# Kernel tuning notes

Measured on AMD Instinct MI355X. Metric: run time of the kernel, lower is better.

Reference implementation:

```python
import jax, jax.numpy as jnp
import numpy as np

B, S, HID = 2, 2048, 2048
NH, NKV, HD = 16, 4, 128
ROT = 64            # head_dim * partial_rotary_factor
WINDOW = 512        # sliding_window_size
ROPE_BASE = 10000.0


def setup_inputs() -> dict:
    key = jax.random.key(0)
    ks = jax.random.split(key, 5)
    scale = 0.02
    return {
        "hidden_states": jax.random.normal(ks[0], (B, S, HID), jnp.float32),
        "Wq": jax.random.normal(ks[1], (NH * HD, HID), jnp.float32) * scale,
        "Wk": jax.random.normal(ks[2], (NKV * HD, HID), jnp.float32) * scale,
        "Wv": jax.random.normal(ks[3], (NKV * HD, HID), jnp.float32) * scale,
        "Wo": jax.random.normal(ks[4], (HID, NH * HD), jnp.float32) * scale,
    }


def _rope_cos_sin(seq_len, dtype):
    inv_freq = 1.0 / (ROPE_BASE ** (jnp.arange(0, ROT, 2, dtype=jnp.float32) / ROT))
    t = jnp.arange(seq_len, dtype=jnp.float32)
    freqs = t[:, None] * inv_freq[None, :]          # [S, ROT/2]
    emb = jnp.concatenate([freqs, freqs], axis=-1)   # [S, ROT]
    return jnp.cos(emb).astype(dtype), jnp.sin(emb).astype(dtype)


def _rotate_half(x):
    x1, x2 = x[..., : x.shape[-1] // 2], x[..., x.shape[-1] // 2:]
    return jnp.concatenate([-x2, x1], axis=-1)


def reference(hidden_states, Wq, Wk, Wv, Wo):
    b, s, _ = hidden_states.shape
    n_rep = NH // NKV

    q = (hidden_states @ Wq.T).reshape(b, s, NH, HD).transpose(0, 2, 1, 3)    # [B,NH,S,HD]
    k = (hidden_states @ Wk.T).reshape(b, s, NKV, HD).transpose(0, 2, 1, 3)   # [B,NKV,S,HD]
    v = (hidden_states @ Wv.T).reshape(b, s, NKV, HD).transpose(0, 2, 1, 3)

    # partial rotary embedding on the first ROT dims
    cos, sin = _rope_cos_sin(s, q.dtype)   # [S, ROT]
    cos = cos[None, None]                  # broadcast over batch, heads
    sin = sin[None, None]
    q_rot, q_pass = q[..., :ROT], q[..., ROT:]
    k_rot, k_pass = k[..., :ROT], k[..., ROT:]
    q_rot = q_rot * cos + _rotate_half(q_rot) * sin
    k_rot = k_rot * cos + _rotate_half(k_rot) * sin
    q = jnp.concatenate([q_rot, q_pass], axis=-1)
    k = jnp.concatenate([k_rot, k_pass], axis=-1)

    # GQA: repeat kv heads
    k = jnp.repeat(k, n_rep, axis=1)   # [B,NH,S,HD]
    v = jnp.repeat(v, n_rep, axis=1)

    scores = jnp.einsum("bhqd,bhkd->bhqk", q, k) / jnp.sqrt(jnp.asarray(HD, q.dtype))

    # sliding-window causal mask: allow j in [i-WINDOW+1, i]
    i = jnp.arange(s)[:, None]
    j = jnp.arange(s)[None, :]
    allowed = (j <= i) & (j > i - WINDOW)
    scores = jnp.where(allowed[None, None], scores, -jnp.inf)

    attn = jax.nn.softmax(scores.astype(jnp.float32), axis=-1).astype(q.dtype)
    out = jnp.einsum("bhqk,bhkd->bhqd", attn, v)          # [B,NH,S,HD]
    out = out.transpose(0, 2, 1, 3).reshape(b, s, NH * HD)
    return out @ Wo.T
```

## Files before the change

### kernel.cpp

```cpp
#include <hip/hip_runtime.h>
#include <cstdint>
#include <cstddef>

typedef __bf16 bf16;
typedef __attribute__((ext_vector_type(8))) __bf16 bf16x8;
typedef __attribute__((ext_vector_type(4))) __bf16 bf16x4;
typedef __attribute__((ext_vector_type(4))) float f32x4;
typedef __attribute__((ext_vector_type(4))) short s16x4;

#define S_LEN   2048
#define WIN     512
#define NH_Q    16
#define NH_KV   4
#define HD_     128
#define NTOK    4096

#define QSCALE_LOG2E 0.12751744561823337f

#if defined(__has_builtin)
#if __has_builtin(__builtin_amdgcn_mfma_f32_16x16x16bf16_1k)
#define HAVE_MFMA16 1
#endif
#endif
#ifndef HAVE_MFMA16
#define HAVE_MFMA16 0
#endif

#define WAIT_VM4   0x0F74
#define WAIT_VM3   0x0F73
#define WAIT_VM2   0x0F72
#define WAIT_VM0   0x0F70
#define WAIT_L0    0xC07F
#define WAIT_L4    0xC47F
#define WAIT_L6    0xC67F
#define WAIT_L10   0xCA7F
#define CFENCE() __asm__ __volatile__("" ::: "memory")

__device__ __forceinline__ void async_copy16(const void* g, void* l) {
  __builtin_amdgcn_global_load_lds(
      (const __attribute__((address_space(1))) void*)g,
      (__attribute__((address_space(3))) void*)l, 16, 0, 0);
}

__global__ __launch_bounds__(256)
void cvt_all(const float* __restrict__ hs, const float* __restrict__ wq,
             const float* __restrict__ wk, const float* __restrict__ wv,
             const float* __restrict__ wo, bf16* __restrict__ hsb,
             bf16* __restrict__ wqb, bf16* __restrict__ wkb,
             bf16* __restrict__ wvb, bf16* __restrict__ wob) {
  long i = ((long)blockIdx.x * 256 + threadIdx.x) * 4;
  const float* in;
  bf16* out;
  if (i < 8388608)       { in = hs + i;            out = hsb + i; }
  else if (i < 12582912) { in = wq + (i - 8388608); out = wqb + (i - 8388608); }
  else if (i < 13631488) { in = wk + (i - 12582912); out = wkb + (i - 12582912); }
  else if (i < 14680064) { in = wv + (i - 13631488); out = wvb + (i - 13631488); }
  else                   { in = wo + (i - 14680064); out = wob + (i - 14680064); }
  float4 v = *(const float4*)in;
  bf16x4 t = {(bf16)v.x, (bf16)v.y, (bf16)v.z, (bf16)v.w};
  *(bf16x4*)out = t;
}

__global__ __launch_bounds__(512, 2)
void gemm_out8(const bf16* __restrict__ A, const bf16* __restrict__ W,
               float* __restrict__ C) {
  __shared__ __align__(16) char smem[98304];
  const int tid  = threadIdx.x;
  const int wave = tid >> 6, lane = tid & 63;
  const int quad = lane >> 4, l16 = lane & 15;
  const int wm = wave >> 1, wn = wave & 1;

  const int flat = blockIdx.y * 16 + blockIdx.x;
  const int swz  = (flat & 7) * 32 + (flat >> 3);
  const int m0 = (swz >> 4) * 256;
  const int n0 = (swz & 15) * 128;

  const int rdb = (l16 * 64 + quad * 16) ^ ((l16 & 8) << 2);
  const int srow = lane >> 2;
  const int scol = ((lane & 3) * 8) ^ ((lane >> 5) << 4);

  const bf16* aptr[2][2];
  int adst[2][2];
#pragma unroll
  for (int mh = 0; mh < 2; ++mh)
#pragma unroll
    for (int j = 0; j < 2; ++j) {
      const int rb = (wave >> 1) * 4 + mh * 2 + j;
      aptr[mh][j] = A + (size_t)(m0 + rb * 16 + srow) * 2048 + scol
                    + (wave & 1) * 32;
      adst[mh][j] = (rb * 2 + (wave & 1)) << 10;
    }
  const bf16* bptr[2];
  int bdst[2];
#pragma unroll
  for (int nh = 0; nh < 2; ++nh) {
    const int cb = (wave >> 2) * 4 + nh * 2 + ((wave >> 1) & 1);
    bptr[nh] = W + (size_t)(n0 + cb * 16 + srow) * 2048 + scol
               + (wave & 1) * 32;
    bdst[nh] = (cb * 2 + (wave & 1)) << 10;
  }

#define STAGE_A(mh, tt) do { char* _b = smem + ((tt) & 1) * 32768;      \
    async_copy16(aptr[mh][0] + (tt) * 64, _b + adst[mh][0]);            \
    async_copy16(aptr[mh][1] + (tt) * 64, _b + adst[mh][1]); } while (0)
#define STAGE_B(nh, tt) do { char* _b = smem + 65536 + ((tt) & 1) * 16384; \
    async_copy16(bptr[nh] + (tt) * 64, _b + bdst[nh]); } while (0)

  f32x4 acc[4][4];
#pragma unroll
  for (int i = 0; i < 4; ++i)
#pragma unroll
    for (int j = 0; j < 4; ++j) acc[i][j] = (f32x4){0.f, 0.f, 0.f, 0.f};

  bf16x8 afr[2][2];
  bf16x8 bfr[2][2][2];

  auto read_a = [&](const char* Ab, int mh) __attribute__((always_inline)) {
#pragma unroll
    for (int mt2 = 0; mt2 < 2; ++mt2)
#pragma unroll
      for (int ks = 0; ks < 2; ++ks)
        afr[mt2][ks] = *(const bf16x8*)(
            Ab + (((wm * 4 + mh * 2 + mt2) * 2 + ks) << 10) + rdb);
  };
  auto read_b = [&](const char* Bb, int nh) __attribute__((always_inline)) {
#pragma unroll
    for (int nt2 = 0; nt2 < 2; ++nt2)
#pragma unroll
      for (int ks = 0; ks < 2; ++ks)
        bfr[nh][nt2][ks] = *(const bf16x8*)(
            Bb + (((wn * 4 + nh * 2 + nt2) * 2 + ks) << 10) + rdb);
  };
  auto do_mfma = [&](int mh, int nh) __attribute__((always_inline)) {
    __builtin_amdgcn_s_setprio(1);
#pragma unroll
    for (int mt2 = 0; mt2 < 2; ++mt2)
#pragma unroll
      for (int nt2 = 0; nt2 < 2; ++nt2)
#pragma unroll
        for (int ks = 0; ks < 2; ++ks)
          acc[mh * 2 + mt2][nh * 2 + nt2] = __builtin_amdgcn_mfma_f32_16x16x32_bf16(
              afr[mt2][ks], bfr[nh][nt2][ks], acc[mh * 2 + mt2][nh * 2 + nt2],
              0, 0, 0);
    __builtin_amdgcn_s_setprio(0);
  };

  STAGE_A(0, 0); STAGE_B(0, 0); STAGE_B(1, 0); STAGE_A(1, 0);
  CFENCE();

  for (int t = 0; t < 31; ++t) {
    const char* Ab = smem + (t & 1) * 32768;
    const char* Bb = smem + 65536 + (t & 1) * 16384;
    const int nx = t + 1;
    __builtin_amdgcn_s_waitcnt(WAIT_VM3); CFENCE();
    __builtin_amdgcn_s_barrier(); CFENCE();
    read_a(Ab, 0); read_b(Bb, 0);
    STAGE_A(0, nx); CFENCE();
    do_mfma(0, 0);
    __builtin_amdgcn_s_waitcnt(WAIT_VM4); CFENCE();
    __builtin_amdgcn_s_barrier(); CFENCE();
    read_b(Bb, 1);
    STAGE_B(0, nx); CFENCE();
    do_mfma(0, 1);
    __builtin_amdgcn_s_waitcnt(WAIT_VM3); CFENCE();
    __builtin_amdgcn_s_barrier(); CFENCE();
    read_a(Ab, 1);
    STAGE_B(1, nx); CFENCE();
    do_mfma(1, 0);
    __builtin_amdgcn_s_barrier(); CFENCE();
    STAGE_A(1, nx); CFENCE();
    do_mfma(1, 1);
  }
  {
    const char* Ab = smem + 32768;
    const char* Bb = smem + 65536 + 16384;
    __builtin_amdgcn_s_waitcnt(WAIT_VM3); CFENCE();
    __builtin_amdgcn_s_barrier(); CFENCE();
    read_a(Ab, 0); read_b(Bb, 0);
    do_mfma(0, 0);
    __builtin_amdgcn_s_waitcnt(WAIT_VM2); CFENCE();
    __builtin_amdgcn_s_barrier(); CFENCE();
    read_b(Bb, 1);
    do_mfma(0, 1);
    __builtin_amdgcn_s_waitcnt(WAIT_VM0); CFENCE();
    __builtin_amdgcn_s_barrier(); CFENCE();
    read_a(Ab, 1);
    do_mfma(1, 0);
    do_mfma(1, 1);
  }
#undef STAGE_A
#undef STAGE_B

#pragma unroll
  for (int mt = 0; mt < 4; ++mt)
#pragma unroll
    for (int nt = 0; nt < 4; ++nt)
#pragma unroll
      for (int r = 0; r < 4; ++r) {
        const int row = m0 + wm * 64 + mt * 16 + quad * 4 + r;
        const int col = n0 + wn * 64 + nt * 16 + l16;
        C[(size_t)row * 2048 + col] = acc[mt][nt][r];
      }
}

__global__ __launch_bounds__(512, 2)
void gemm_qkv10(const bf16* __restrict__ A, const bf16* __restrict__ Wq,
                const bf16* __restrict__ Wk, const bf16* __restrict__ Wv,
                bf16* __restrict__ Qo, bf16* __restrict__ Ko,
                bf16* __restrict__ Vt) {
  __shared__ __align__(16) char smem[114688];
  const int tid  = threadIdx.x;
  const int wave = tid >> 6, lane = tid & 63;
  const int quad = lane >> 4, l16 = lane & 15;
  const int wm = wave >> 1, wn = wave & 1;

  const int flat = blockIdx.y * 16 + blockIdx.x;
  const int swz  = (flat & 7) * 32 + (flat >> 3);
  const int m0 = (swz >> 4) * 256;
  const int n0 = (swz & 15) * 192;

  const int rdb = (l16 * 64 + quad * 16) ^ ((l16 & 8) << 2);
  const int srow = lane >> 2;
  const int scol = ((lane & 3) * 8) ^ ((lane >> 5) << 4);

  const int rbA0 = (wave >> 1) * 4 + (wave & 1);
  const int rbA1 = rbA0 + 2;
  const bf16* a0p = A + (size_t)(m0 + rbA0 * 16 + srow) * 2048 + scol;
  const bf16* a1p = A + (size_t)(m0 + rbA1 * 16 + srow) * 2048 + scol;
  const int da0 = (rbA0 * 2) << 10;
  const int da1 = (rbA1 * 2) << 10;

  const int rbB0 = wave >> 1, khB0 = wave & 1;
  const int rbB1 = 4 + wave;
  const int nrow0 = n0 + rbB0 * 16 + srow;
  const int nrow1 = n0 + rbB1 * 16 + srow;
  const bf16* b0p = (nrow0 < 2048 ? Wq + (size_t)nrow0 * 2048
                   : nrow0 < 2560 ? Wk + (size_t)(nrow0 - 2048) * 2048
                                  : Wv + (size_t)(nrow0 - 2560) * 2048)
                    + scol + khB0 * 32;
  const bf16* b1p = (nrow1 < 2048 ? Wq + (size_t)nrow1 * 2048
                   : nrow1 < 2560 ? Wk + (size_t)(nrow1 - 2048) * 2048
                                  : Wv + (size_t)(nrow1 - 2560) * 2048)
                    + scol;
  const int db0 = (rbB0 * 2 + khB0) << 10;
  const int db1 = (rbB1 * 2) << 10;

#define STAGE_A0(tt) do { char* _b = smem + ((tt) & 1) * 32768;        \
    async_copy16(a0p + (tt) * 64,      _b + da0);                      \
    async_copy16(a0p + (tt) * 64 + 32, _b + da0 + 1024); } while (0)
#define STAGE_A1(tt) do { char* _b = smem + ((tt) & 1) * 32768;        \
    async_copy16(a1p + (tt) * 64,      _b + da1);                      \
    async_copy16(a1p + (tt) * 64 + 32, _b + da1 + 1024); } while (0)
#define STAGE_B0(tt) do { char* _b = smem + 65536 + ((tt) & 1) * 24576; \
    async_copy16(b0p + (tt) * 64,      _b + db0); } while (0)
#define STAGE_B12(tt) do { char* _b = smem + 65536 + ((tt) & 1) * 24576; \
    async_copy16(b1p + (tt) * 64,      _b + db1);                      \
    async_copy16(b1p + (tt) * 64 + 32, _b + db1 + 1024); } while (0)

  f32x4 acc[4][6];
#pragma unroll
  for (int i = 0; i < 4; ++i)
#pragma unroll
    for (int j = 0; j < 6; ++j) acc[i][j] = (f32x4){0.f, 0.f, 0.f, 0.f};

  bf16x8 afr0[2][2];
  bf16x8 afr1[2][2];
  bf16x8 bfr[6][2];

  auto read_a0 = [&](const char* Ab) __attribute__((always_inline)) {
#pragma unroll
    for (int mt2 = 0; mt2 < 2; ++mt2)
#pragma unroll
      for (int ks = 0; ks < 2; ++ks)
        afr0[mt2][ks] = *(const bf16x8*)(
            Ab + (((wm * 4 + mt2) * 2 + ks) << 10) + rdb);
  };
  auto read_a1 = [&](const char* Ab) __attribute__((always_inline)) {
#pragma unroll
    for (int mt2 = 0; mt2 < 2; ++mt2)
#pragma unroll
      for (int ks = 0; ks < 2; ++ks)
        afr1[mt2][ks] = *(const bf16x8*)(
            Ab + (((wm * 4 + 2 + mt2) * 2 + ks) << 10) + rdb);
  };
  auto read_b_ks = [&](const char* Bb, int ks) __attribute__((always_inline)) {
#pragma unroll
    for (int j = 0; j < 6; ++j) {
      const int cc = (j >> 1) * 4 + (j & 1) * 2 + wn;
      bfr[j][ks] = *(const bf16x8*)(Bb + ((cc * 2 + ks) << 10) + rdb);
    }
  };
  auto mfma0 = [&](int ks) __attribute__((always_inline)) {
    __builtin_amdgcn_s_setprio(1);
#pragma unroll
    for (int mt2 = 0; mt2 < 2; ++mt2)
#pragma unroll
      for (int j = 0; j < 6; ++j)
        acc[mt2][j] = __builtin_amdgcn_mfma_f32_16x16x32_bf16(
            afr0[mt2][ks], bfr[j][ks], acc[mt2][j], 0, 0, 0);
    __builtin_amdgcn_s_setprio(0);
  };
  auto mfma1 = [&](int ks) __attribute__((always_inline)) {
    __builtin_amdgcn_s_setprio(1);
#pragma unroll
    for (int mt2 = 0; mt2 < 2; ++mt2)
#pragma unroll
      for (int j = 0; j < 6; ++j)
        acc[2 + mt2][j] = __builtin_amdgcn_mfma_f32_16x16x32_bf16(
            afr1[mt2][ks], bfr[j][ks], acc[2 + mt2][j], 0, 0, 0);
    __builtin_amdgcn_s_setprio(0);
  };

  STAGE_A0(0); STAGE_B0(0); STAGE_B12(0); STAGE_A1(0);
  CFENCE();
  __builtin_amdgcn_s_waitcnt(WAIT_VM0); CFENCE();
  __builtin_amdgcn_s_barrier(); CFENCE();
  read_a0(smem);
  read_b_ks(smem + 65536, 0);
  CFENCE();

  for (int t = 0; t < 31; ++t) {
    const char* Ab  = smem + (t & 1) * 32768;
    const char* Bb  = smem + 65536 + (t & 1) * 24576;
    const char* Abn = smem + ((t + 1) & 1) * 32768;
    const char* Bbn = smem + 65536 + ((t + 1) & 1) * 24576;
    const int nx = t + 1;
    __builtin_amdgcn_s_barrier(); CFENCE();
    read_b_ks(Bb, 1);
    STAGE_A0(nx); CFENCE();
    __builtin_amdgcn_s_waitcnt(WAIT_L6);
    __builtin_amdgcn_sched_barrier(0);
    mfma0(0);
    __builtin_amdgcn_s_waitcnt(WAIT_VM2); CFENCE();
    __builtin_amdgcn_s_barrier(); CFENCE();
    read_a1(Ab);
    STAGE_B0(nx); STAGE_B12(nx); CFENCE();
    __builtin_amdgcn_s_waitcnt(WAIT_L4);
    __builtin_amdgcn_sched_barrier(0);
    mfma0(1);
    __builtin_amdgcn_s_barrier(); CFENCE();
    STAGE_A1(nx); CFENCE();
    __builtin_amdgcn_s_waitcnt(WAIT_L0);
    __builtin_amdgcn_sched_barrier(0);
    mfma1(0);
    __builtin_amdgcn_s_waitcnt(WAIT_VM2); CFENCE();
    __builtin_amdgcn_s_barrier(); CFENCE();
    read_a0(Abn);
    read_b_ks(Bbn, 0);
    CFENCE();
    __builtin_amdgcn_s_waitcnt(WAIT_L10);
    __builtin_amdgcn_sched_barrier(0);
    mfma1(1);
  }
  {
    const char* Ab = smem + 32768;
    const char* Bb = smem + 65536 + 24576;
    __builtin_amdgcn_s_barrier(); CFENCE();
    read_b_ks(Bb, 1); CFENCE();
    __builtin_amdgcn_s_waitcnt(WAIT_L6);
    __builtin_amdgcn_sched_barrier(0);
    mfma0(0);
    __builtin_amdgcn_s_waitcnt(WAIT_VM0); CFENCE();
    __builtin_amdgcn_s_barrier(); CFENCE();
    read_a1(Ab); CFENCE();
    __builtin_amdgcn_s_waitcnt(WAIT_L4);
    __builtin_amdgcn_sched_barrier(0);
    mfma0(1);
    __builtin_amdgcn_s_waitcnt(WAIT_L0);
    __builtin_amdgcn_sched_barrier(0);
    mfma1(0);
    mfma1(1);
  }
#undef STAGE_A0
#undef STAGE_A1
#undef STAGE_B0
#undef STAGE_B12

  {
    const float d = (float)(wn * 16 + l16);
    const float invf = exp2f(-d * 0.41524101186091903f);
#pragma unroll
    for (int b = 0; b < 3; ++b) {
      const int cb = n0 + b * 64;
      if (cb < 2560 && (cb & 127) == 0) {
#pragma unroll
        for (int mt = 0; mt < 4; ++mt)
#pragma unroll
          for (int r = 0; r < 4; ++r) {
            const int pos = (m0 + wm * 64 + mt * 16 + quad * 4 + r) & (S_LEN - 1);
            float s, c;
            __sincosf((float)pos * invf, &s, &c);
            const float x1 = acc[mt][2 * b][r], x2 = acc[mt][2 * b + 1][r];
            acc[mt][2 * b][r]     = x1 * c - x2 * s;
            acc[mt][2 * b + 1][r] = x2 * c + x1 * s;
          }
      }
    }
  }
#pragma unroll
  for (int mt = 0; mt < 4; ++mt) {
    const int row0 = m0 + wm * 64 + mt * 16 + quad * 4;
#pragma unroll
    for (int j = 0; j < 6; ++j) {
      const int col16 = n0 + (j >> 1) * 64 + ((j & 1) * 2 + wn) * 16;
      if (col16 < 2048) {
#pragma unroll
        for (int r = 0; r < 4; ++r)
          Qo[(size_t)(row0 + r) * 2048 + col16 + l16] =
              (bf16)(acc[mt][j][r] * QSCALE_LOG2E);
      } else if (col16 < 2560) {
#pragma unroll
        for (int r = 0; r < 4; ++r)
          Ko[(size_t)(row0 + r) * 512 + col16 - 2048 + l16] = (bf16)acc[mt][j][r];
      } else {
        const int colv = col16 + l16 - 2560;
        const int bb = row0 >> 11, s0 = row0 & (S_LEN - 1);
        bf16x4 tq = {(bf16)acc[mt][j][0], (bf16)acc[mt][j][1],
                     (bf16)acc[mt][j][2], (bf16)acc[mt][j][3]};
        *(bf16x4*)(Vt + ((size_t)(bb * NH_KV + (colv >> 7)) * HD_ + (colv & 127))
                        * S_LEN + s0) = tq;
      }
    }
  }
}

#define KS_STRIDE 136
#define VT_STRIDE 72

__global__ __launch_bounds__(512, 4)
void attn_kernel(const bf16* __restrict__ Qg, const bf16* __restrict__ Kg,
                 const bf16* __restrict__ Vtg, bf16* __restrict__ Og) {
  __shared__ __align__(16) char smem_raw[35840];
  bf16* const Ks = (bf16*)smem_raw;
  bf16* const Vt = (bf16*)(smem_raw + 17408);
  bf16* const Os = (bf16*)smem_raw;

  const int tid  = threadIdx.x;
  const int wave = tid >> 6, lane = tid & 63;
  const int quad = lane >> 4, l16 = lane & 15;

  const int flat = blockIdx.x + 16 * blockIdx.y + 256 * blockIdx.z;
  const int swz  = (flat & 7) * 64 + (flat >> 3);
  const int qt = swz & 15, h = (swz >> 4) & 15, b = swz >> 8;

  const int kv = h >> 2;
  const int q0 = qt * 128;
  const int tok0 = b * S_LEN;
  const int qw = q0 + wave * 16;
  const int q  = qw + l16;

  bf16x8 qf[4];
  {
    const bf16* qp = Qg + (size_t)(tok0 + q) * (NH_Q * HD_) + h * HD_ + quad * 8;
#pragma unroll
    for (int kb = 0; kb < 4; ++kb) qf[kb] = *(const bf16x8*)(qp + kb * 32);
  }

  f32x4 o[8];
#pragma unroll
  for (int dt = 0; dt < 8; ++dt) o[dt] = (f32x4){0.f, 0.f, 0.f, 0.f};
  float m_run = -__builtin_inff(), l_run = 0.f;

  int kt_begin = q0 - WIN;
  if (kt_begin < 0) kt_begin = 0;
  const int kt_end = q0 + 128;
  const bf16* kg_base = Kg + (size_t)tok0 * (NH_KV * HD_) + kv * HD_;
  const bf16* vt_base = Vtg + (size_t)(b * NH_KV + kv) * HD_ * S_LEN;

  const int skey = tid >> 4, sdbl = tid & 15;
  const int svd  = tid >> 3, skb  = tid & 7;

  bf16x8 pk0, pk1, pv0, pv1;
  auto PF = [&](int kt) __attribute__((always_inline)) {
    pk0 = *(const bf16x8*)(kg_base + (size_t)(kt + skey) * (NH_KV * HD_) + sdbl * 8);
    pk1 = *(const bf16x8*)(kg_base + (size_t)(kt + skey + 32) * (NH_KV * HD_) + sdbl * 8);
    pv0 = *(const bf16x8*)(vt_base + (size_t)svd * S_LEN + kt + skb * 8);
    pv1 = *(const bf16x8*)(vt_base + (size_t)(svd + 64) * S_LEN + kt + skb * 8);
  };
  auto WR = [&]() __attribute__((always_inline)) {
    *(bf16x8*)&Ks[skey * KS_STRIDE + sdbl * 8] = pk0;
    *(bf16x8*)&Ks[(skey + 32) * KS_STRIDE + sdbl * 8] = pk1;
    *(bf16x8*)&Vt[svd * VT_STRIDE + skb * 8] = pv0;
    *(bf16x8*)&Vt[(svd + 64) * VT_STRIDE + skb * 8] = pv1;
  };

  PF(kt_begin);
  for (int kt = kt_begin; kt < kt_end; kt += 64) {
    __syncthreads();
    WR();
    __syncthreads();
    if (kt + 64 < kt_end) PF(kt + 64);

    const bool active = (kt <= qw + 15) && (kt + 63 > qw - WIN);
    if (!active) continue;
    const bool need_c = (kt + 63 > qw);
    const bool need_l = (kt + WIN <= qw + 15);

    f32x4 st4[4];
    __builtin_amdgcn_s_setprio(1);
#pragma unroll
    for (int nt = 0; nt < 4; ++nt) {
      f32x4 acc = (f32x4){0.f, 0.f, 0.f, 0.f};
#pragma unroll
      for (int kb = 0; kb < 4; ++kb) {
        bf16x8 kf = *(const bf16x8*)&Ks[(nt * 16 + l16) * KS_STRIDE + kb * 32 + quad * 8];
        acc = __builtin_amdgcn_mfma_f32_16x16x32_bf16(kf, qf[kb], acc, 0, 0, 0);
      }
      st4[nt] = acc;
    }
    __builtin_amdgcn_s_setprio(0);

    if (need_c || need_l) {
#pragma unroll
      for (int nt = 0; nt < 4; ++nt)
#pragma unroll
        for (int r = 0; r < 4; ++r) {
          const int key = kt + nt * 16 + quad * 4 + r;
          const bool ok = (!need_c || key <= q) && (!need_l || key > q - WIN);
          st4[nt][r] = ok ? st4[nt][r] : -__builtin_inff();
        }
    }

    float mx = -__builtin_inff();
#pragma unroll
    for (int nt = 0; nt < 4; ++nt)
#pragma unroll
      for (int r = 0; r < 4; ++r) mx = fmaxf(mx, st4[nt][r]);
    mx = fmaxf(mx, __shfl_xor(mx, 16, 64));
    mx = fmaxf(mx, __shfl_xor(mx, 32, 64));

    float msub;
    if (!__all(mx - m_run <= 8.f)) {
      const float mnew = fmaxf(m_run, mx);
      msub = (mnew == -__builtin_inff()) ? 0.f : mnew;
      const float alpha = __builtin_amdgcn_exp2f(m_run - msub);
      l_run *= alpha;
#pragma unroll
      for (int dt = 0; dt < 8; ++dt) o[dt] *= alpha;
      m_run = mnew;
    } else {
      msub = m_run;
    }

    float psum = 0.f;
    s16x4 pb[4];
#pragma unroll
    for (int nt = 0; nt < 4; ++nt)
#pragma unroll
      for (int r = 0; r < 4; ++r) {
        const float pv = __builtin_amdgcn_exp2f(st4[nt][r] - msub);
        psum += pv;
        union { __bf16 hh; short ss; } u;
        u.hh = (bf16)pv;
        pb[nt][r] = u.ss;
      }
    psum += __shfl_xor(psum, 16, 64);
    psum += __shfl_xor(psum, 32, 64);
    l_run += psum;

    __builtin_amdgcn_s_setprio(1);
#pragma unroll
    for (int dt = 0; dt < 8; ++dt)
#pragma unroll
      for (int nt = 0; nt < 4; ++nt) {
        s16x4 vf = *(const s16x4*)&Vt[(dt * 16 + l16) * VT_STRIDE + nt * 16 + quad * 4];
        o[dt] = __builtin_amdgcn_mfma_f32_16x16x16bf16_1k(vf, pb[nt], o[dt], 0, 0, 0);
      }
    __builtin_amdgcn_s_setprio(0);
  }

  const float inv = 1.f / l_run;
  __syncthreads();
#pragma unroll
  for (int dt = 0; dt < 8; ++dt) {
    bf16x4 t;
#pragma unroll
    for (int r = 0; r < 4; ++r) t[r] = (bf16)(o[dt][r] * inv);
    *(bf16x4*)&Os[(wave * 16 + l16) * KS_STRIDE + dt * 16 + quad * 4] = t;
  }
  __syncthreads();
#pragma unroll
  for (int it = 0; it < 4; ++it) {
    const int idx = tid + it * 512;
    const int row = idx >> 4, chunk = idx & 15;
    bf16x8 v = *(const bf16x8*)&Os[row * KS_STRIDE + chunk * 8];
    *(bf16x8*)(Og + (size_t)(tok0 + q0 + row) * (NH_Q * HD_) + h * HD_ + chunk * 8) = v;
  }
}

extern "C" void kernel_launch(void* const* d_in, const int* in_sizes, int n_in,
                              void* d_out, int out_size, void* d_ws, size_t ws_size,
                              hipStream_t stream) {
  const float* hs = (const float*)d_in[0];
  const float* Wq = (const float*)d_in[1];
  const float* Wk = (const float*)d_in[2];
  const float* Wv = (const float*)d_in[3];
  const float* Wo = (const float*)d_in[4];
  float* out = (float*)d_out;

  char* w = (char*)d_ws;
  bf16* hsb = (bf16*)w; w += (size_t)NTOK * 2048 * 2;
  bf16* wqb = (bf16*)w; w += (size_t)2048 * 2048 * 2;
  bf16* wkb = (bf16*)w; w += (size_t)512 * 2048 * 2;
  bf16* wvb = (bf16*)w; w += (size_t)512 * 2048 * 2;
  bf16* wob = (bf16*)w; w += (size_t)2048 * 2048 * 2;
  bf16* qb  = (bf16*)w; w += (size_t)NTOK * 2048 * 2;
  bf16* kb  = (bf16*)w; w += (size_t)NTOK * 512 * 2;
  bf16* vtb = (bf16*)w; w += (size_t)NTOK * 512 * 2;
  bf16* ab  = hsb;

  cvt_all<<<18874368 / 1024, 256, 0, stream>>>(hs, Wq, Wk, Wv, Wo,
                                               hsb, wqb, wkb, wvb, wob);

  gemm_qkv10<<<dim3(16, 16), 512, 0, stream>>>(hsb, wqb, wkb, wvb,
                                               qb, kb, vtb);

  attn_kernel<<<dim3(S_LEN / 128, NH_Q, 2), 512, 0, stream>>>(qb, kb, vtb, ab);

  gemm_out8<<<dim3(16, 16), 512, 0, stream>>>(ab, wob, out);
}
```

Baseline: 233.1 us.

## Restructure QKV GEMM to 4-stage K32 pipeline with prefetch distance three

Reworks the QKV projection GEMM main loop. It now runs 64 K-steps of 32 through a 4-deep ring of LDS buffers instead of 32 steps of 64 through a double buffer. Global-to-LDS async loads are issued three steps ahead, and each step is split into two MFMA phases, each guarded by a barrier. The aim is to hide global load latency more deeply. The cost is more barriers per unit of work and a more complex per-wave vmcnt wait scheme.

```diff
diff --git a/kernel.cpp b/kernel.cpp
--- a/kernel.cpp
+++ b/kernel.cpp
@@ -26,14 +26,13 @@
 #define HAVE_MFMA16 0
 #endif
 
+#define WAIT_VM8   0x0F78
+#define WAIT_VM6   0x0F76
 #define WAIT_VM4   0x0F74
 #define WAIT_VM3   0x0F73
 #define WAIT_VM2   0x0F72
 #define WAIT_VM0   0x0F70
 #define WAIT_L0    0xC07F
-#define WAIT_L4    0xC47F
-#define WAIT_L6    0xC67F
-#define WAIT_L10   0xCA7F
 #define CFENCE() __asm__ __volatile__("" ::: "memory")
 
 __device__ __forceinline__ void async_copy16(const void* g, void* l) {
@@ -204,7 +203,7 @@
 }
 
 __global__ __launch_bounds__(512, 2)
-void gemm_qkv10(const bf16* __restrict__ A, const bf16* __restrict__ Wq,
+void gemm_qkv11(const bf16* __restrict__ A, const bf16* __restrict__ Wq,
                 const bf16* __restrict__ Wk, const bf16* __restrict__ Wv,
                 bf16* __restrict__ Qo, bf16* __restrict__ Ko,
                 bf16* __restrict__ Vt) {
@@ -223,39 +222,37 @@
   const int srow = lane >> 2;
   const int scol = ((lane & 3) * 8) ^ ((lane >> 5) << 4);
 
-  const int rbA0 = (wave >> 1) * 4 + (wave & 1);
-  const int rbA1 = rbA0 + 2;
-  const bf16* a0p = A + (size_t)(m0 + rbA0 * 16 + srow) * 2048 + scol;
-  const bf16* a1p = A + (size_t)(m0 + rbA1 * 16 + srow) * 2048 + scol;
-  const int da0 = (rbA0 * 2) << 10;
-  const int da1 = (rbA1 * 2) << 10;
-
-  const int rbB0 = wave >> 1, khB0 = wave & 1;
-  const int rbB1 = 4 + wave;
-  const int nrow0 = n0 + rbB0 * 16 + srow;
-  const int nrow1 = n0 + rbB1 * 16 + srow;
-  const bf16* b0p = (nrow0 < 2048 ? Wq + (size_t)nrow0 * 2048
-                   : nrow0 < 2560 ? Wk + (size_t)(nrow0 - 2048) * 2048
-                                  : Wv + (size_t)(nrow0 - 2560) * 2048)
-                    + scol + khB0 * 32;
-  const bf16* b1p = (nrow1 < 2048 ? Wq + (size_t)nrow1 * 2048
-                   : nrow1 < 2560 ? Wk + (size_t)(nrow1 - 2048) * 2048
-                                  : Wv + (size_t)(nrow1 - 2560) * 2048)
-                    + scol;
-  const int db0 = (rbB0 * 2 + khB0) << 10;
-  const int db1 = (rbB1 * 2) << 10;
-
-#define STAGE_A0(tt) do { char* _b = smem + ((tt) & 1) * 32768;        \
-    async_copy16(a0p + (tt) * 64,      _b + da0);                      \
-    async_copy16(a0p + (tt) * 64 + 32, _b + da0 + 1024); } while (0)
-#define STAGE_A1(tt) do { char* _b = smem + ((tt) & 1) * 32768;        \
-    async_copy16(a1p + (tt) * 64,      _b + da1);                      \
-    async_copy16(a1p + (tt) * 64 + 32, _b + da1 + 1024); } while (0)
-#define STAGE_B0(tt) do { char* _b = smem + 65536 + ((tt) & 1) * 24576; \
-    async_copy16(b0p + (tt) * 64,      _b + db0); } while (0)
-#define STAGE_B12(tt) do { char* _b = smem + 65536 + ((tt) & 1) * 24576; \
-    async_copy16(b1p + (tt) * 64,      _b + db1);                      \
-    async_copy16(b1p + (tt) * 64 + 32, _b + db1 + 1024); } while (0)
+  const bf16* aup[2];
+  int adst[2];
+#pragma unroll
+  for (int i = 0; i < 2; ++i) {
+    const int uA = wave * 2 + i;
+    aup[i]  = A + (size_t)(m0 + uA * 16 + srow) * 2048 + scol;
+    adst[i] = uA << 10;
+  }
+  const int uB0 = (wave < 4) ? wave * 2 : 4 + wave;
+  const int uB1 = wave * 2 + 1;
+  const int nrow0 = n0 + uB0 * 16 + srow;
+  const int nrow1 = n0 + uB1 * 16 + srow;
+  const bf16* bup0 = (nrow0 < 2048 ? Wq + (size_t)nrow0 * 2048
+                    : nrow0 < 2560 ? Wk + (size_t)(nrow0 - 2048) * 2048
+                                   : Wv + (size_t)(nrow0 - 2560) * 2048) + scol;
+  const bf16* bup1 = (nrow1 < 2048 ? Wq + (size_t)nrow1 * 2048
+                    : nrow1 < 2560 ? Wk + (size_t)(nrow1 - 2048) * 2048
+                                   : Wv + (size_t)(nrow1 - 2560) * 2048) + scol;
+  const int bdst0 = uB0 << 10;
+  const int bdst1 = uB1 << 10;
+
+  auto stageA = [&](int tt) __attribute__((always_inline)) {
+    char* _b = smem + (tt & 3) * 16384;
+    async_copy16(aup[0] + (size_t)tt * 32, _b + adst[0]);
+    async_copy16(aup[1] + (size_t)tt * 32, _b + adst[1]);
+  };
+  auto stageB = [&](int tt) __attribute__((always_inline)) {
+    char* _b = smem + 65536 + (tt & 3) * 12288;
+    async_copy16(bup0 + (size_t)tt * 32, _b + bdst0);
+    if (wave < 4) async_copy16(bup1 + (size_t)tt * 32, _b + bdst1);
+  };
 
   f32x4 acc[4][6];
 #pragma unroll
@@ -263,118 +260,111 @@
 #pragma unroll
     for (int j = 0; j < 6; ++j) acc[i][j] = (f32x4){0.f, 0.f, 0.f, 0.f};
 
-  bf16x8 afr0[2][2];
-  bf16x8 afr1[2][2];
-  bf16x8 bfr[6][2];
-
-  auto read_a0 = [&](const char* Ab) __attribute__((always_inline)) {
+  bf16x8 afr[2], afr2[2];
+  bf16x8 bfr[6];
+
+  auto read_ph1 = [&](int t) __attribute__((always_inline)) {
+    const char* sA = smem + (t & 3) * 16384;
+    const char* sB = smem + 65536 + (t & 3) * 12288;
 #pragma unroll
     for (int mt2 = 0; mt2 < 2; ++mt2)
-#pragma unroll
-      for (int ks = 0; ks < 2; ++ks)
-        afr0[mt2][ks] = *(const bf16x8*)(
-            Ab + (((wm * 4 + mt2) * 2 + ks) << 10) + rdb);
-  };
-  auto read_a1 = [&](const char* Ab) __attribute__((always_inline)) {
-#pragma unroll
-    for (int mt2 = 0; mt2 < 2; ++mt2)
-#pragma unroll
-      for (int ks = 0; ks < 2; ++ks)
-        afr1[mt2][ks] = *(const bf16x8*)(
-            Ab + (((wm * 4 + 2 + mt2) * 2 + ks) << 10) + rdb);
-  };
-  auto read_b_ks = [&](const char* Bb, int ks) __attribute__((always_inline)) {
+      afr[mt2] = *(const bf16x8*)(sA + ((wm * 4 + mt2) << 10) + rdb);
 #pragma unroll
     for (int j = 0; j < 6; ++j) {
       const int cc = (j >> 1) * 4 + (j & 1) * 2 + wn;
-      bfr[j][ks] = *(const bf16x8*)(Bb + ((cc * 2 + ks) << 10) + rdb);
+      bfr[j] = *(const bf16x8*)(sB + (cc << 10) + rdb);
     }
   };
-  auto mfma0 = [&](int ks) __attribute__((always_inline)) {
+  auto read_ph2 = [&](int t) __attribute__((always_inline)) {
+    const char* sA = smem + (t & 3) * 16384;
+#pragma unroll
+    for (int mt2 = 0; mt2 < 2; ++mt2)
+      afr2[mt2] = *(const bf16x8*)(sA + ((wm * 4 + 2 + mt2) << 10) + rdb);
+  };
+  auto mfma_ph1 = [&]() __attribute__((always_inline)) {
     __builtin_amdgcn_s_setprio(1);
 #pragma unroll
     for (int mt2 = 0; mt2 < 2; ++mt2)
 #pragma unroll
       for (int j = 0; j < 6; ++j)
         acc[mt2][j] = __builtin_amdgcn_mfma_f32_16x16x32_bf16(
-            afr0[mt2][ks], bfr[j][ks], acc[mt2][j], 0, 0, 0);
+            afr[mt2], bfr[j], acc[mt2][j], 0, 0, 0);
     __builtin_amdgcn_s_setprio(0);
   };
-  auto mfma1 = [&](int ks) __attribute__((always_inline)) {
+  auto mfma_ph2 = [&]() __attribute__((always_inline)) {
     __builtin_amdgcn_s_setprio(1);
 #pragma unroll
     for (int mt2 = 0; mt2 < 2; ++mt2)
 #pragma unroll
       for (int j = 0; j < 6; ++j)
         acc[2 + mt2][j] = __builtin_amdgcn_mfma_f32_16x16x32_bf16(
-            afr1[mt2][ks], bfr[j][ks], acc[2 + mt2][j], 0, 0, 0);
+            afr2[mt2], bfr[j], acc[2 + mt2][j], 0, 0, 0);
     __builtin_amdgcn_s_setprio(0);
   };
 
-  STAGE_A0(0); STAGE_B0(0); STAGE_B12(0); STAGE_A1(0);
+  stageA(0); stageB(0);
+  stageA(1); stageB(1);
+  stageA(2); stageB(2);
   CFENCE();
-  __builtin_amdgcn_s_waitcnt(WAIT_VM0); CFENCE();
+  if (wave < 4) __builtin_amdgcn_s_waitcnt(WAIT_VM8);
+  else          __builtin_amdgcn_s_waitcnt(WAIT_VM6);
+  CFENCE();
   __builtin_amdgcn_s_barrier(); CFENCE();
-  read_a0(smem);
-  read_b_ks(smem + 65536, 0);
-  CFENCE();
-
-  for (int t = 0; t < 31; ++t) {
-    const char* Ab  = smem + (t & 1) * 32768;
-    const char* Bb  = smem + 65536 + (t & 1) * 24576;
-    const char* Abn = smem + ((t + 1) & 1) * 32768;
-    const char* Bbn = smem + 65536 + ((t + 1) & 1) * 24576;
-    const int nx = t + 1;
-    __builtin_amdgcn_s_barrier(); CFENCE();
-    read_b_ks(Bb, 1);
-    STAGE_A0(nx); CFENCE();
-    __builtin_amdgcn_s_waitcnt(WAIT_L6);
-    __builtin_amdgcn_sched_barrier(0);
-    mfma0(0);
-    __builtin_amdgcn_s_waitcnt(WAIT_VM2); CFENCE();
-    __builtin_amdgcn_s_barrier(); CFENCE();
-    read_a1(Ab);
-    STAGE_B0(nx); STAGE_B12(nx); CFENCE();
-    __builtin_amdgcn_s_waitcnt(WAIT_L4);
-    __builtin_amdgcn_sched_barrier(0);
-    mfma0(1);
-    __builtin_amdgcn_s_barrier(); CFENCE();
-    STAGE_A1(nx); CFENCE();
-    __builtin_amdgcn_s_waitcnt(WAIT_L0);
-    __builtin_amdgcn_sched_barrier(0);
-    mfma1(0);
-    __builtin_amdgcn_s_waitcnt(WAIT_VM2); CFENCE();
-    __builtin_amdgcn_s_barrier(); CFENCE();
-    read_a0(Abn);
-    read_b_ks(Bbn, 0);
+
+  for (int t = 0; t < 61; ++t) {
+    read_ph1(t);
+    stageA(t + 3);
     CFENCE();
-    __builtin_amdgcn_s_waitcnt(WAIT_L10);
-    __builtin_amdgcn_sched_barrier(0);
-    mfma1(1);
+    __builtin_amdgcn_s_barrier(); CFENCE();
+    __builtin_amdgcn_s_waitcnt(WAIT_L0);
+    __builtin_amdgcn_sched_barrier(0);
+    mfma_ph1();
+    read_ph2(t);
+    stageB(t + 3);
+    CFENCE();
+    if (wave < 4) __builtin_amdgcn_s_waitcnt(WAIT_VM8);
+    else          __builtin_amdgcn_s_waitcnt(WAIT_VM6);
+    CFENCE();
+    __builtin_amdgcn_s_barrier(); CFENCE();
+    __builtin_amdgcn_s_waitcnt(WAIT_L0);
+    __builtin_amdgcn_sched_barrier(0);
+    mfma_ph2();
   }
   {
-    const char* Ab = smem + 32768;
-    const char* Bb = smem + 65536 + 24576;
-    __builtin_amdgcn_s_barrier(); CFENCE();
-    read_b_ks(Bb, 1); CFENCE();
-    __builtin_amdgcn_s_waitcnt(WAIT_L6);
-    __builtin_amdgcn_sched_barrier(0);
-    mfma0(0);
+    read_ph1(61); CFENCE();
+    __builtin_amdgcn_s_barrier(); CFENCE();
+    __builtin_amdgcn_s_waitcnt(WAIT_L0);
+    __builtin_amdgcn_sched_barrier(0);
+    mfma_ph1();
+    read_ph2(61); CFENCE();
+    if (wave < 4) __builtin_amdgcn_s_waitcnt(WAIT_VM4);
+    else          __builtin_amdgcn_s_waitcnt(WAIT_VM3);
+    CFENCE();
+    __builtin_amdgcn_s_barrier(); CFENCE();
+    __builtin_amdgcn_s_waitcnt(WAIT_L0);
+    __builtin_amdgcn_sched_barrier(0);
+    mfma_ph2();
+    read_ph1(62); CFENCE();
+    __builtin_amdgcn_s_barrier(); CFENCE();
+    __builtin_amdgcn_s_waitcnt(WAIT_L0);
+    __builtin_amdgcn_sched_barrier(0);
+    mfma_ph1();
+    read_ph2(62); CFENCE();
     __builtin_amdgcn_s_waitcnt(WAIT_VM0); CFENCE();
     __builtin_amdgcn_s_barrier(); CFENCE();
-    read_a1(Ab); CFENCE();
-    __builtin_amdgcn_s_waitcnt(WAIT_L4);
-    __builtin_amdgcn_sched_barrier(0);
-    mfma0(1);
-    __builtin_amdgcn_s_waitcnt(WAIT_L0);
-    __builtin_amdgcn_sched_barrier(0);
-    mfma1(0);
-    mfma1(1);
-  }
-#undef STAGE_A0
-#undef STAGE_A1
-#undef STAGE_B0
-#undef STAGE_B12
+    __builtin_amdgcn_s_waitcnt(WAIT_L0);
+    __builtin_amdgcn_sched_barrier(0);
+    mfma_ph2();
+    read_ph1(63); CFENCE();
+    __builtin_amdgcn_s_barrier(); CFENCE();
+    __builtin_amdgcn_s_waitcnt(WAIT_L0);
+    __builtin_amdgcn_sched_barrier(0);
+    mfma_ph1();
+    read_ph2(63); CFENCE();
+    __builtin_amdgcn_s_waitcnt(WAIT_L0);
+    __builtin_amdgcn_sched_barrier(0);
+    mfma_ph2();
+  }
 
   {
     const float d = (float)(wn * 16 + l16);
@@ -612,7 +602,7 @@
   cvt_all<<<18874368 / 1024, 256, 0, stream>>>(hs, Wq, Wk, Wv, Wo,
                                                hsb, wqb, wkb, wvb, wob);
 
-  gemm_qkv10<<<dim3(16, 16), 512, 0, stream>>>(hsb, wqb, wkb, wvb,
+  gemm_qkv11<<<dim3(16, 16), 512, 0, stream>>>(hsb, wqb, wkb, wvb,
                                                qb, kb, vtb);
 
   attn_kernel<<<dim3(S_LEN / 128, NH_Q, 2), 512, 0, stream>>>(qb, kb, vtb, ab);
```

Measured after the change: 238.7 us. 1.02x slower.
